# Kernel tuning notes

Hardware: AMD Instinct MI355X
Metric: run time of the kernel (lower is better)

Reference implementation:

```python
import jax, jax.numpy as jnp
import numpy as np

D = 384      # n_embed_dims
H = 6        # n_heads
HS = D // H  # head_size = 64
T = 256      # block_size
B = 256
EPS = 1e-5


def setup_inputs() -> dict:
    key = jax.random.key(0)
    ks = jax.random.split(key, 12)
    s_in = 1.0 / np.sqrt(D)
    s_ff = 1.0 / np.sqrt(4 * D)
    return {
        "x": jax.random.normal(ks[0], (B, T, D), jnp.float32),
        # per-head QKV weights, stacked [H, D, HS] (Linear bias=False)
        "wq": jax.random.normal(ks[1], (H, D, HS), jnp.float32) * s_in,
        "wk": jax.random.normal(ks[2], (H, D, HS), jnp.float32) * s_in,
        "wv": jax.random.normal(ks[3], (H, D, HS), jnp.float32) * s_in,
        "w_proj": jax.random.normal(ks[4], (D, D), jnp.float32) * s_in,
        "b_proj": jax.random.normal(ks[5], (D,), jnp.float32) * s_in,
        "w1": jax.random.normal(ks[6], (D, 4 * D), jnp.float32) * s_in,
        "b1": jax.random.normal(ks[7], (4 * D,), jnp.float32) * s_in,
        "w2": jax.random.normal(ks[8], (4 * D, D), jnp.float32) * s_ff,
        "b2": jax.random.normal(ks[9], (D,), jnp.float32) * s_ff,
        "g1": jnp.ones((D,), jnp.float32),
        "be1": jnp.zeros((D,), jnp.float32),
        "g2": jnp.ones((D,), jnp.float32),
        "be2": jnp.zeros((D,), jnp.float32),
    }


def _layernorm(x, g, b):
    mu = jnp.mean(x, axis=-1, keepdims=True)
    var = jnp.mean(jnp.square(x - mu), axis=-1, keepdims=True)
    return (x - mu) * jax.lax.rsqrt(var + EPS) * g + b


def _attention(x, wq, wk, wv, w_proj, b_proj):
    # faithful quirk: scale = 1/sqrt(C) with C = full embed dim (384)
    scale = 1.0 / jnp.sqrt(jnp.asarray(D, x.dtype))
    q = jnp.einsum("btd,hde->bhte", x, wq)  # [B,H,T,HS]
    k = jnp.einsum("btd,hde->bhte", x, wk)
    v = jnp.einsum("btd,hde->bhte", x, wv)
    w = jnp.einsum("bhte,bhse->bhts", q, k) * scale  # [B,H,T,T], no mask
    w = jax.nn.softmax(w, axis=-1)
    out = jnp.einsum("bhts,bhse->bhte", w, v)  # [B,H,T,HS]
    # concat heads along feature dim (head order matches torch cat)
    out = out.transpose(0, 2, 1, 3).reshape(x.shape[0], x.shape[1], D)
    return out @ w_proj + b_proj


def reference(x, wq, wk, wv, w_proj, b_proj, w1, b1, w2, b2, g1, be1, g2, be2):
    x = x + _attention(_layernorm(x, g1, be1), wq, wk, wv, w_proj, b_proj)
    h = _layernorm(x, g2, be2)
    h = jax.nn.relu(h @ w1 + b1) @ w2 + b2  # dropout = eval-mode identity
    return x + h
```

## Files before the change

### kernel.cpp

```cpp
#include <hip/hip_runtime.h>
#include <stdint.h>

#define NTOK 65536
#define DE 384
#define QSTR 1280

typedef __bf16 bf16x8 __attribute__((ext_vector_type(8)));
typedef float  f32x4 __attribute__((ext_vector_type(4)));
typedef unsigned short u16x8 __attribute__((ext_vector_type(8)));

__device__ __forceinline__ unsigned short f2bf(float f) {
  union { float fl; unsigned u; } a; a.fl = f;
  unsigned r = a.u + 0x7fffu + ((a.u >> 16) & 1u);
  return (unsigned short)(r >> 16);
}
__device__ __forceinline__ float b2f(unsigned short s) {
  union { unsigned u; float f; } v; v.u = (unsigned)s << 16; return v.f;
}

__device__ __forceinline__ void gll16(const void* g, void* l) {
  __builtin_amdgcn_global_load_lds((const __attribute__((address_space(1))) void*)g,
                                   (__attribute__((address_space(3))) void*)l, 16, 0, 0);
}

__device__ __forceinline__ bf16x8 ds128(unsigned addr) {
  bf16x8 r;
  asm volatile("ds_read_b128 %0, %1" : "=v"(r) : "v"(addr));
  return r;
}

__global__ void pack_t(unsigned short* __restrict__ dst, const float* __restrict__ src,
                       int R, int C) {
  int t = blockIdx.x * 256 + threadIdx.x;
  if (t >= R * C) return;
  int r = t / C, c = t - r * C;
  dst[(size_t)c * R + r] = f2bf(src[t]);
}

__global__ void qkv_pack(const float* __restrict__ wq, const float* __restrict__ wk,
                         const float* __restrict__ wv, unsigned short* __restrict__ dst) {
  int t = blockIdx.x * 256 + threadIdx.x;
  if (t >= QSTR * 384) return;
  int n = t / 384, k = t - n * 384;
  unsigned short v = 0;
  if (n < 1152) {
    int which = n / 384, r = n - which * 384;
    const float* src = which == 0 ? wq : (which == 1 ? wk : wv);
    int h = r >> 6, e = r & 63;
    v = f2bf(src[h * 24576 + k * 64 + e]);
  }
  dst[t] = v;
}

__global__ __launch_bounds__(256) void ln_kernel(const float* __restrict__ x,
                                                 const float* __restrict__ g,
                                                 const float* __restrict__ be,
                                                 unsigned short* __restrict__ out) {
  int wave = threadIdx.x >> 6, lane = threadIdx.x & 63;
  size_t row = (size_t)blockIdx.x * 4 + wave;
  const float* xr = x + row * DE;
  int c0 = lane * 2;
  float2 v0 = *(const float2*)(xr + c0);
  float2 v1 = *(const float2*)(xr + 128 + c0);
  float2 v2 = *(const float2*)(xr + 256 + c0);
  float s  = v0.x + v0.y + v1.x + v1.y + v2.x + v2.y;
  float ss = v0.x*v0.x + v0.y*v0.y + v1.x*v1.x + v1.y*v1.y + v2.x*v2.x + v2.y*v2.y;
#pragma unroll
  for (int m = 1; m < 64; m <<= 1) { s += __shfl_xor(s, m); ss += __shfl_xor(ss, m); }
  float mu = s * (1.0f / 384.0f);
  float rstd = rsqrtf(ss * (1.0f / 384.0f) - mu * mu + 1e-5f);
  unsigned short* orow = out + row * DE;
  {
    float a0 = (v0.x - mu) * rstd * g[c0] + be[c0];
    float a1 = (v0.y - mu) * rstd * g[c0 + 1] + be[c0 + 1];
    *(unsigned*)(orow + c0) = (unsigned)f2bf(a0) | ((unsigned)f2bf(a1) << 16);
  }
  {
    int c = c0 + 128;
    float a0 = (v1.x - mu) * rstd * g[c] + be[c];
    float a1 = (v1.y - mu) * rstd * g[c + 1] + be[c + 1];
    *(unsigned*)(orow + c) = (unsigned)f2bf(a0) | ((unsigned)f2bf(a1) << 16);
  }
  {
    int c = c0 + 256;
    float a0 = (v2.x - mu) * rstd * g[c] + be[c];
    float a1 = (v2.y - mu) * rstd * g[c + 1] + be[c + 1];
    *(unsigned*)(orow + c) = (unsigned)f2bf(a0) | ((unsigned)f2bf(a1) << 16);
  }
}

__global__ __launch_bounds__(256) void ln_bf16(const unsigned short* __restrict__ x,
                                               const float* __restrict__ g,
                                               const float* __restrict__ be,
                                               unsigned short* __restrict__ out) {
  int wave = threadIdx.x >> 6, lane = threadIdx.x & 63;
  size_t row = (size_t)blockIdx.x * 4 + wave;
  const unsigned short* xr = x + row * DE;
  int c0 = lane * 2;
  unsigned u0 = *(const unsigned*)(xr + c0);
  unsigned u1 = *(const unsigned*)(xr + 128 + c0);
  unsigned u2 = *(const unsigned*)(xr + 256 + c0);
  float a0 = b2f((unsigned short)u0), a1 = b2f((unsigned short)(u0 >> 16));
  float b0 = b2f((unsigned short)u1), b1 = b2f((unsigned short)(u1 >> 16));
  float d0 = b2f((unsigned short)u2), d1 = b2f((unsigned short)(u2 >> 16));
  float s  = a0 + a1 + b0 + b1 + d0 + d1;
  float ss = a0*a0 + a1*a1 + b0*b0 + b1*b1 + d0*d0 + d1*d1;
#pragma unroll
  for (int m = 1; m < 64; m <<= 1) { s += __shfl_xor(s, m); ss += __shfl_xor(ss, m); }
  float mu = s * (1.0f / 384.0f);
  float rstd = rsqrtf(ss * (1.0f / 384.0f) - mu * mu + 1e-5f);
  unsigned short* orow = out + row * DE;
  {
    float r0 = (a0 - mu) * rstd * g[c0] + be[c0];
    float r1 = (a1 - mu) * rstd * g[c0 + 1] + be[c0 + 1];
    *(unsigned*)(orow + c0) = (unsigned)f2bf(r0) | ((unsigned)f2bf(r1) << 16);
  }
  {
    int c = c0 + 128;
    float r0 = (b0 - mu) * rstd * g[c] + be[c];
    float r1 = (b1 - mu) * rstd * g[c + 1] + be[c + 1];
    *(unsigned*)(orow + c) = (unsigned)f2bf(r0) | ((unsigned)f2bf(r1) << 16);
  }
  {
    int c = c0 + 256;
    float r0 = (d0 - mu) * rstd * g[c] + be[c];
    float r1 = (d1 - mu) * rstd * g[c + 1] + be[c + 1];
    *(unsigned*)(orow + c) = (unsigned)f2bf(r0) | ((unsigned)f2bf(r1) << 16);
  }
}

template<int EPI, int BM, int BN, int WM, int WN>
__device__ __forceinline__
void gemm_core(const unsigned short* __restrict__ A, const unsigned short* __restrict__ Bt,
               int M, int Ncmp, int K, int Nst, int stride, int ntx,
               const float* __restrict__ bias, const float* __restrict__ residf,
               const unsigned short* __restrict__ residb,
               float* __restrict__ outf, unsigned short* __restrict__ outb) {
  constexpr int T = WM * WN * 64;
  constexpr int MWT = BM / WM, NWT = BN / WN;
  constexpr int MF = MWT / 16, NF = NWT / 16;
  constexpr int MH = MF / 4;
  constexpr int LA = (BM * 128) / (T * 16);
  constexpr int LB = (BN * 128) / (T * 16);
  __shared__ __align__(16) unsigned short As[2][BM * 64];
  __shared__ __align__(16) unsigned short Bs[2][BN * 64];
  const int tid = threadIdx.x;
  const int wave = tid >> 6, lane = tid & 63;

  const int nwg = gridDim.x;
  const int cpx = nwg >> 3;
  const int wg = (blockIdx.x & 7) * cpx + (blockIdx.x >> 3);
  const int bx = wg % ntx, by = wg / ntx;
  const int mBase = by * BM, nBase = bx * BN;
  const int wmi = wave / WN, wni = wave % WN;
  const int wm = wmi * MWT, wn = wni * NWT;
  const int fr = lane & 15, fg = lane >> 4;

  const unsigned asb = (unsigned)(uintptr_t)&As[0][0];
  const unsigned bsb = (unsigned)(uintptr_t)&Bs[0][0];

  f32x4 acc[MF][NF];
  const f32x4 z = {0.f, 0.f, 0.f, 0.f};
#pragma unroll
  for (int i = 0; i < MF; ++i)
#pragma unroll
    for (int j = 0; j < NF; ++j) acc[i][j] = z;

  auto stage = [&](int buf, int kt) {
#pragma unroll
    for (int i = 0; i < LA; ++i) {
      int Lb = i * (T * 16) + wave * 1024;
      int L = Lb + lane * 16;
      int row = L >> 7;
      int col = (((L >> 4) & 7) ^ (row & 7)) << 3;
      gll16(A + (size_t)(mBase + row) * K + kt + col, (unsigned short*)As[buf] + (Lb >> 1));
    }
#pragma unroll
    for (int i = 0; i < LB; ++i) {
      int Lb = i * (T * 16) + wave * 1024;
      int L = Lb + lane * 16;
      int row = L >> 7;
      int col = (((L >> 4) & 7) ^ (row & 7)) << 3;
      gll16(Bt + (size_t)(nBase + row) * K + kt + col, (unsigned short*)Bs[buf] + (Lb >> 1));
    }
  };

  const int NK = K >> 6;
  stage(0, 0);
  for (int t = 0; t < NK; ++t) {
    const int cur = t & 1;
    if (t + 1 < NK) {
      stage(cur ^ 1, (t + 1) << 6);
      if constexpr (LA + LB == 8) asm volatile("s_waitcnt vmcnt(8)" ::: "memory");
      else                        asm volatile("s_waitcnt vmcnt(6)" ::: "memory");
    } else {
      asm volatile("s_waitcnt vmcnt(0)" ::: "memory");
    }
    asm volatile("" ::: "memory");
    __builtin_amdgcn_s_barrier();
    asm volatile("" ::: "memory");

    const unsigned ab = asb + (cur ? (unsigned)(BM * 128) : 0u);
    const unsigned bb = bsb + (cur ? (unsigned)(BN * 128) : 0u);
#pragma unroll
    for (int ks = 0; ks < 2; ++ks) {
      bf16x8 bfr[NF];
#pragma unroll
      for (int nb = 0; nb < NF; ++nb) {
        int row = wn + nb * 16 + fr;
        unsigned byte = (unsigned)(row << 7) + ((unsigned)((ks * 4 + fg) ^ (row & 7)) << 4);
        bfr[nb] = ds128(bb + byte);
      }
#pragma unroll
      for (int mh = 0; mh < MH; ++mh) {
        bf16x8 af[4];
#pragma unroll
        for (int mb = 0; mb < 4; ++mb) {
          int row = wm + (mh * 4 + mb) * 16 + fr;
          unsigned byte = (unsigned)(row << 7) + ((unsigned)((ks * 4 + fg) ^ (row & 7)) << 4);
          af[mb] = ds128(ab + byte);
        }
        asm volatile("s_waitcnt lgkmcnt(0)" ::: "memory");
        __builtin_amdgcn_sched_barrier(0);
        __builtin_amdgcn_s_setprio(1);
#pragma unroll
        for (int mb = 0; mb < 4; ++mb)
#pragma unroll
          for (int nb = 0; nb < NF; ++nb)
            acc[mh * 4 + mb][nb] =
                __builtin_amdgcn_mfma_f32_16x16x32_bf16(af[mb], bfr[nb], acc[mh * 4 + mb][nb], 0, 0, 0);
        __builtin_amdgcn_s_setprio(0);
      }
    }
    asm volatile("" ::: "memory");
    __builtin_amdgcn_s_barrier();
    asm volatile("" ::: "memory");
  }

#pragma unroll
  for (int mb = 0; mb < MF; ++mb) {
#pragma unroll
    for (int nb = 0; nb < NF; ++nb) {
      const int gn = nBase + wn + nb * 16 + fr;
      if (gn < Nst) {
#pragma unroll
        for (int i = 0; i < 4; ++i) {
          const int gm = mBase + wm + mb * 16 + (fg << 2) + i;
          float val = acc[mb][nb][i];
          size_t idx = (size_t)gm * stride + gn;
          if (EPI == 0) {
            outb[idx] = f2bf(val);
          } else if (EPI == 1) {
            outb[idx] = f2bf(val + bias[gn] + residf[idx]);
          } else if (EPI == 2) {
            float r = val + bias[gn];
            outb[idx] = f2bf(r > 0.f ? r : 0.f);
          } else {
            outf[idx] = val + bias[gn] + b2f(residb[idx]);
          }
        }
      }
    }
  }
}

__global__ __launch_bounds__(512, 1)
void gemm_qkv(const unsigned short* __restrict__ A, const unsigned short* __restrict__ Bt,
              int M, int Ncmp, int K, int Nst, int stride, int ntx,
              const float* __restrict__ bias, const float* __restrict__ residf,
              const unsigned short* __restrict__ residb, float* __restrict__ outf,
              unsigned short* __restrict__ outb) {
  gemm_core<0, 256, 256, 2, 4>(A, Bt, M, Ncmp, K, Nst, stride, ntx, bias, residf, residb, outf, outb);
}
__global__ __launch_bounds__(512, 1)
void gemm_proj(const unsigned short* __restrict__ A, const unsigned short* __restrict__ Bt,
               int M, int Ncmp, int K, int Nst, int stride, int ntx,
               const float* __restrict__ bias, const float* __restrict__ residf,
               const unsigned short* __restrict__ residb, float* __restrict__ outf,
               unsigned short* __restrict__ outb) {
  gemm_core<1, 256, 128, 4, 2>(A, Bt, M, Ncmp, K, Nst, stride, ntx, bias, residf, residb, outf, outb);
}
__global__ __launch_bounds__(512, 1)
void gemm_mlp1(const unsigned short* __restrict__ A, const unsigned short* __restrict__ Bt,
               int M, int Ncmp, int K, int Nst, int stride, int ntx,
               const float* __restrict__ bias, const float* __restrict__ residf,
               const unsigned short* __restrict__ residb, float* __restrict__ outf,
               unsigned short* __restrict__ outb) {
  gemm_core<2, 256, 256, 2, 4>(A, Bt, M, Ncmp, K, Nst, stride, ntx, bias, residf, residb, outf, outb);
}
__global__ __launch_bounds__(512, 1)
void gemm_mlp2(const unsigned short* __restrict__ A, const unsigned short* __restrict__ Bt,
               int M, int Ncmp, int K, int Nst, int stride, int ntx,
               const float* __restrict__ bias, const float* __restrict__ residf,
               const unsigned short* __restrict__ residb, float* __restrict__ outf,
               unsigned short* __restrict__ outb) {
  gemm_core<3, 256, 128, 4, 2>(A, Bt, M, Ncmp, K, Nst, stride, ntx, bias, residf, residb, outf, outb);
}

__global__ __launch_bounds__(256)
void attn_kernel(const unsigned short* __restrict__ qkvn, unsigned short* __restrict__ o) {
  __shared__ unsigned short Vt[64 * 256];
  __shared__ unsigned short Pw[4][64 * 32];
  const int bh = blockIdx.x;
  const int b = bh / 6, h = bh - b * 6;
  const unsigned short* base = qkvn + (size_t)(b * 256) * QSTR;
  const unsigned short* qb = base + h * 64;
  const unsigned short* kbp = base + 384 + h * 64;
  const unsigned short* vbp = base + 768 + h * 64;
  const int wave = threadIdx.x >> 6, lane = threadIdx.x & 63;
  const int fr = lane & 15, fg = lane >> 4;
  const int fk = fg << 3;
  const int qrow0 = wave << 6;
  const float scale = 0.051031036307982884f;
  const f32x4 z = {0.f, 0.f, 0.f, 0.f};

  {
    const int s = threadIdx.x;
    u16x8 v8[8];
#pragma unroll
    for (int j = 0; j < 8; ++j)
      v8[j] = *(const u16x8*)(vbp + (size_t)s * QSTR + j * 8);
#pragma unroll
    for (int e = 0; e < 64; ++e)
      Vt[(e << 8) + (s ^ ((e & 7) << 3))] = v8[e >> 3][e & 7];
  }
  __syncthreads();

  bf16x8 qf[4][2];
#pragma unroll
  for (int rb = 0; rb < 4; ++rb)
#pragma unroll
    for (int ks = 0; ks < 2; ++ks)
      qf[rb][ks] = *(const bf16x8*)(qb + (size_t)(qrow0 + rb * 16 + fr) * QSTR + ks * 32 + fk);

  f32x4 oacc[4][4];
  float psum[4][4];
#pragma unroll
  for (int rb = 0; rb < 4; ++rb)
#pragma unroll
    for (int nb = 0; nb < 4; ++nb) oacc[rb][nb] = z;
#pragma unroll
  for (int rb = 0; rb < 4; ++rb)
#pragma unroll
    for (int i = 0; i < 4; ++i) psum[rb][i] = 0.f;

  for (int kb2 = 0; kb2 < 8; ++kb2) {
#pragma unroll
    for (int c2 = 0; c2 < 2; ++c2) {
      int cb = kb2 * 2 + c2;
      bf16x8 kf0 = *(const bf16x8*)(kbp + (size_t)(cb * 16 + fr) * QSTR + fk);
      bf16x8 kf1 = *(const bf16x8*)(kbp + (size_t)(cb * 16 + fr) * QSTR + 32 + fk);
#pragma unroll
      for (int rb = 0; rb < 4; ++rb) {
        f32x4 s = __builtin_amdgcn_mfma_f32_16x16x32_bf16(qf[rb][0], kf0, z, 0, 0, 0);
        s = __builtin_amdgcn_mfma_f32_16x16x32_bf16(qf[rb][1], kf1, s, 0, 0, 0);
#pragma unroll
        for (int i = 0; i < 4; ++i) {
          float p = __expf(fminf(scale * s[i], 60.f));
          psum[rb][i] += p;
          Pw[wave][(rb * 16 + (fg << 2) + i) * 32 + c2 * 16 + fr] = f2bf(p);
        }
      }
    }
    bf16x8 pa[4], vf[4];
#pragma unroll
    for (int rb = 0; rb < 4; ++rb) pa[rb] = *(const bf16x8*)(&Pw[wave][(rb * 16 + fr) * 32 + fk]);
#pragma unroll
    for (int nb = 0; nb < 4; ++nb) {
      int e = nb * 16 + fr;
      vf[nb] = *(const bf16x8*)(&Vt[(e << 8) + ((kb2 * 32 + fk) ^ ((e & 7) << 3))]);
    }
#pragma unroll
    for (int rb = 0; rb < 4; ++rb)
#pragma unroll
      for (int nb = 0; nb < 4; ++nb)
        oacc[rb][nb] = __builtin_amdgcn_mfma_f32_16x16x32_bf16(pa[rb], vf[nb], oacc[rb][nb], 0, 0, 0);
  }

  float rs[4][4];
#pragma unroll
  for (int rb = 0; rb < 4; ++rb)
#pragma unroll
    for (int i = 0; i < 4; ++i) {
      float v = psum[rb][i];
      v += __shfl_xor(v, 1);
      v += __shfl_xor(v, 2);
      v += __shfl_xor(v, 4);
      v += __shfl_xor(v, 8);
      rs[rb][i] = 1.0f / v;
    }

#pragma unroll
  for (int rb = 0; rb < 4; ++rb)
#pragma unroll
    for (int nb = 0; nb < 4; ++nb)
#pragma unroll
      for (int i = 0; i < 4; ++i) {
        int token = b * 256 + qrow0 + rb * 16 + (fg << 2) + i;
        int gcol = h * 64 + nb * 16 + fr;
        o[(size_t)token * DE + gcol] = f2bf(oacc[rb][nb][i] * rs[rb][i]);
      }
}

extern "C" void kernel_launch(void* const* d_in, const int* in_sizes, int n_in,
                              void* d_out, int out_size, void* d_ws, size_t ws_size,
                              hipStream_t stream) {
  const float* x     = (const float*)d_in[0];
  const float* wq    = (const float*)d_in[1];
  const float* wk    = (const float*)d_in[2];
  const float* wv    = (const float*)d_in[3];
  const float* wproj = (const float*)d_in[4];
  const float* bproj = (const float*)d_in[5];
  const float* w1    = (const float*)d_in[6];
  const float* b1    = (const float*)d_in[7];
  const float* w2    = (const float*)d_in[8];
  const float* b2    = (const float*)d_in[9];
  const float* g1    = (const float*)d_in[10];
  const float* be1   = (const float*)d_in[11];
  const float* g2    = (const float*)d_in[12];
  const float* be2   = (const float*)d_in[13];

  char* ws = (char*)d_ws;
  unsigned short* xln   = (unsigned short*)(ws + 0);
  unsigned short* x1b   = (unsigned short*)(ws + 0);
  unsigned short* qkvn  = (unsigned short*)(ws + 50331648);
  unsigned short* hbuf  = (unsigned short*)(ws + 100663296);
  unsigned short* act   = (unsigned short*)(ws + 150994944);
  unsigned short* attno = (unsigned short*)(ws + 218103808);
  unsigned short* wqkvt = (unsigned short*)(ws + 352321536);
  unsigned short* wprjt = (unsigned short*)(ws + 352321536 + 983040);
  unsigned short* w1t   = (unsigned short*)(ws + 352321536 + 983040 + 294912);
  unsigned short* w2t   = (unsigned short*)(ws + 352321536 + 983040 + 294912 + 1179648);

  qkv_pack<<<(QSTR * 384 + 255) / 256, 256, 0, stream>>>(wq, wk, wv, wqkvt);
  pack_t<<<(147456 + 255) / 256, 256, 0, stream>>>(wprjt, wproj, 384, 384);
  pack_t<<<(589824 + 255) / 256, 256, 0, stream>>>(w1t, w1, 384, 1536);
  pack_t<<<(589824 + 255) / 256, 256, 0, stream>>>(w2t, w2, 1536, 384);

  ln_kernel<<<NTOK / 4, 256, 0, stream>>>(x, g1, be1, xln);

  gemm_qkv<<<5 * 256, 512, 0, stream>>>(xln, wqkvt, NTOK, 1280, 384, 1152, 1280, 5,
                                        nullptr, nullptr, nullptr, nullptr, qkvn);

  attn_kernel<<<1536, 256, 0, stream>>>(qkvn, attno);

  gemm_proj<<<3 * 256, 512, 0, stream>>>(attno, wprjt, NTOK, 384, 384, 384, 384, 3,
                                         bproj, x, nullptr, nullptr, x1b);

  ln_bf16<<<NTOK / 4, 256, 0, stream>>>(x1b, g2, be2, hbuf);

  gemm_mlp1<<<6 * 256, 512, 0, stream>>>(hbuf, w1t, NTOK, 1536, 384, 1536, 1536, 6,
                                         b1, nullptr, nullptr, nullptr, act);

  gemm_mlp2<<<3 * 256, 512, 0, stream>>>(act, w2t, NTOK, 384, 1536, 384, 384, 3,
                                         b2, nullptr, x1b, (float*)d_out, nullptr);
}
```

Measured before the change: 544.4 us.

## Fuse second LayerNorm into projection GEMM epilogue and retile QKV GEMM

The projection GEMM now uses full-row tiles (BM=128, BN=384), so each workgroup holds complete rows. It adds bias and residual, computes the row mean and variance through shuffles and a shared-memory reduction, and writes both x1 and the LayerNorm-2 output. This removes the separate ln_bf16 kernel and its extra read of x1. The QKV GEMM tile width also changes from 256 to 192 columns, with 6 column tiles covering exactly 1152 instead of padding to 1280. In exchange, the projection grid drops to 512 workgroups with larger per-workgroup tiles, which risks lower occupancy and register pressure.

```diff
diff --git a/kernel.cpp b/kernel.cpp
--- a/kernel.cpp
+++ b/kernel.cpp
@@ -89,53 +89,15 @@
   }
 }
 
-__global__ __launch_bounds__(256) void ln_bf16(const unsigned short* __restrict__ x,
-                                               const float* __restrict__ g,
-                                               const float* __restrict__ be,
-                                               unsigned short* __restrict__ out) {
-  int wave = threadIdx.x >> 6, lane = threadIdx.x & 63;
-  size_t row = (size_t)blockIdx.x * 4 + wave;
-  const unsigned short* xr = x + row * DE;
-  int c0 = lane * 2;
-  unsigned u0 = *(const unsigned*)(xr + c0);
-  unsigned u1 = *(const unsigned*)(xr + 128 + c0);
-  unsigned u2 = *(const unsigned*)(xr + 256 + c0);
-  float a0 = b2f((unsigned short)u0), a1 = b2f((unsigned short)(u0 >> 16));
-  float b0 = b2f((unsigned short)u1), b1 = b2f((unsigned short)(u1 >> 16));
-  float d0 = b2f((unsigned short)u2), d1 = b2f((unsigned short)(u2 >> 16));
-  float s  = a0 + a1 + b0 + b1 + d0 + d1;
-  float ss = a0*a0 + a1*a1 + b0*b0 + b1*b1 + d0*d0 + d1*d1;
-#pragma unroll
-  for (int m = 1; m < 64; m <<= 1) { s += __shfl_xor(s, m); ss += __shfl_xor(ss, m); }
-  float mu = s * (1.0f / 384.0f);
-  float rstd = rsqrtf(ss * (1.0f / 384.0f) - mu * mu + 1e-5f);
-  unsigned short* orow = out + row * DE;
-  {
-    float r0 = (a0 - mu) * rstd * g[c0] + be[c0];
-    float r1 = (a1 - mu) * rstd * g[c0 + 1] + be[c0 + 1];
-    *(unsigned*)(orow + c0) = (unsigned)f2bf(r0) | ((unsigned)f2bf(r1) << 16);
-  }
-  {
-    int c = c0 + 128;
-    float r0 = (b0 - mu) * rstd * g[c] + be[c];
-    float r1 = (b1 - mu) * rstd * g[c + 1] + be[c + 1];
-    *(unsigned*)(orow + c) = (unsigned)f2bf(r0) | ((unsigned)f2bf(r1) << 16);
-  }
-  {
-    int c = c0 + 256;
-    float r0 = (d0 - mu) * rstd * g[c] + be[c];
-    float r1 = (d1 - mu) * rstd * g[c + 1] + be[c + 1];
-    *(unsigned*)(orow + c) = (unsigned)f2bf(r0) | ((unsigned)f2bf(r1) << 16);
-  }
-}
-
 template<int EPI, int BM, int BN, int WM, int WN>
 __device__ __forceinline__
 void gemm_core(const unsigned short* __restrict__ A, const unsigned short* __restrict__ Bt,
-               int M, int Ncmp, int K, int Nst, int stride, int ntx,
+               int M, int K, int Nst, int stride, int ntx,
                const float* __restrict__ bias, const float* __restrict__ residf,
                const unsigned short* __restrict__ residb,
-               float* __restrict__ outf, unsigned short* __restrict__ outb) {
+               const float* __restrict__ g2, const float* __restrict__ be2,
+               float* __restrict__ outf, unsigned short* __restrict__ outb,
+               unsigned short* __restrict__ out2) {
   constexpr int T = WM * WN * 64;
   constexpr int MWT = BM / WM, NWT = BN / WN;
   constexpr int MF = MWT / 16, NF = NWT / 16;
@@ -144,6 +106,7 @@
   constexpr int LB = (BN * 128) / (T * 16);
   __shared__ __align__(16) unsigned short As[2][BM * 64];
   __shared__ __align__(16) unsigned short Bs[2][BN * 64];
+  __shared__ float red[BM][4][2];
   const int tid = threadIdx.x;
   const int wave = tid >> 6, lane = tid & 63;
 
@@ -191,8 +154,9 @@
     const int cur = t & 1;
     if (t + 1 < NK) {
       stage(cur ^ 1, (t + 1) << 6);
-      if constexpr (LA + LB == 8) asm volatile("s_waitcnt vmcnt(8)" ::: "memory");
-      else                        asm volatile("s_waitcnt vmcnt(6)" ::: "memory");
+      if constexpr (LA + LB == 8)      asm volatile("s_waitcnt vmcnt(8)" ::: "memory");
+      else if constexpr (LA + LB == 7) asm volatile("s_waitcnt vmcnt(7)" ::: "memory");
+      else                             asm volatile("s_waitcnt vmcnt(6)" ::: "memory");
     } else {
       asm volatile("s_waitcnt vmcnt(0)" ::: "memory");
     }
@@ -235,6 +199,65 @@
     asm volatile("" ::: "memory");
     __builtin_amdgcn_s_barrier();
     asm volatile("" ::: "memory");
+  }
+
+  if (EPI == 1) {
+#pragma unroll
+    for (int mb = 0; mb < MF; ++mb) {
+#pragma unroll
+      for (int nb = 0; nb < NF; ++nb) {
+        const int gn = nBase + wn + nb * 16 + fr;
+#pragma unroll
+        for (int i = 0; i < 4; ++i) {
+          const int gm = mBase + wm + mb * 16 + (fg << 2) + i;
+          size_t idx = (size_t)gm * stride + gn;
+          acc[mb][nb][i] = acc[mb][nb][i] + bias[gn] + residf[idx];
+        }
+      }
+    }
+#pragma unroll
+    for (int mb = 0; mb < MF; ++mb) {
+#pragma unroll
+      for (int i = 0; i < 4; ++i) {
+        float s = 0.f, ss = 0.f;
+#pragma unroll
+        for (int nb = 0; nb < NF; ++nb) {
+          float v = acc[mb][nb][i];
+          s += v; ss += v * v;
+        }
+        s += __shfl_xor(s, 1); ss += __shfl_xor(ss, 1);
+        s += __shfl_xor(s, 2); ss += __shfl_xor(ss, 2);
+        s += __shfl_xor(s, 4); ss += __shfl_xor(ss, 4);
+        s += __shfl_xor(s, 8); ss += __shfl_xor(ss, 8);
+        if (fr == 0) {
+          int row = wm + mb * 16 + (fg << 2) + i;
+          red[row][wni][0] = s;
+          red[row][wni][1] = ss;
+        }
+      }
+    }
+    __syncthreads();
+#pragma unroll
+    for (int mb = 0; mb < MF; ++mb) {
+#pragma unroll
+      for (int i = 0; i < 4; ++i) {
+        int row = wm + mb * 16 + (fg << 2) + i;
+        float s = red[row][0][0] + red[row][1][0] + red[row][2][0] + red[row][3][0];
+        float ss = red[row][0][1] + red[row][1][1] + red[row][2][1] + red[row][3][1];
+        float mu = s * (1.0f / 384.0f);
+        float rstd = rsqrtf(ss * (1.0f / 384.0f) - mu * mu + 1e-5f);
+        const int gm = mBase + row;
+#pragma unroll
+        for (int nb = 0; nb < NF; ++nb) {
+          const int gn = nBase + wn + nb * 16 + fr;
+          size_t idx = (size_t)gm * stride + gn;
+          float x1v = acc[mb][nb][i];
+          outb[idx] = f2bf(x1v);
+          out2[idx] = f2bf((x1v - mu) * rstd * g2[gn] + be2[gn]);
+        }
+      }
+    }
+    return;
   }
 
 #pragma unroll
@@ -250,8 +273,6 @@
           size_t idx = (size_t)gm * stride + gn;
           if (EPI == 0) {
             outb[idx] = f2bf(val);
-          } else if (EPI == 1) {
-            outb[idx] = f2bf(val + bias[gn] + residf[idx]);
           } else if (EPI == 2) {
             float r = val + bias[gn];
             outb[idx] = f2bf(r > 0.f ? r : 0.f);
@@ -266,35 +287,39 @@
 
 __global__ __launch_bounds__(512, 1)
 void gemm_qkv(const unsigned short* __restrict__ A, const unsigned short* __restrict__ Bt,
-              int M, int Ncmp, int K, int Nst, int stride, int ntx,
+              int M, int K, int Nst, int stride, int ntx,
               const float* __restrict__ bias, const float* __restrict__ residf,
               const unsigned short* __restrict__ residb, float* __restrict__ outf,
               unsigned short* __restrict__ outb) {
-  gemm_core<0, 256, 256, 2, 4>(A, Bt, M, Ncmp, K, Nst, stride, ntx, bias, residf, residb, outf, outb);
+  gemm_core<0, 256, 192, 2, 4>(A, Bt, M, K, Nst, stride, ntx, bias, residf, residb,
+                               nullptr, nullptr, outf, outb, nullptr);
 }
 __global__ __launch_bounds__(512, 1)
-void gemm_proj(const unsigned short* __restrict__ A, const unsigned short* __restrict__ Bt,
-               int M, int Ncmp, int K, int Nst, int stride, int ntx,
+void gemm_projln(const unsigned short* __restrict__ A, const unsigned short* __restrict__ Bt,
+                 int M, int K, int Nst, int stride, int ntx,
+                 const float* __restrict__ bias, const float* __restrict__ residf,
+                 const float* __restrict__ g2, const float* __restrict__ be2,
+                 unsigned short* __restrict__ outb, unsigned short* __restrict__ out2) {
+  gemm_core<1, 128, 384, 2, 4>(A, Bt, M, K, Nst, stride, ntx, bias, residf, nullptr,
+                               g2, be2, nullptr, outb, out2);
+}
+__global__ __launch_bounds__(512, 1)
+void gemm_mlp1(const unsigned short* __restrict__ A, const unsigned short* __restrict__ Bt,
+               int M, int K, int Nst, int stride, int ntx,
                const float* __restrict__ bias, const float* __restrict__ residf,
                const unsigned short* __restrict__ residb, float* __restrict__ outf,
                unsigned short* __restrict__ outb) {
-  gemm_core<1, 256, 128, 4, 2>(A, Bt, M, Ncmp, K, Nst, stride, ntx, bias, residf, residb, outf, outb);
+  gemm_core<2, 256, 256, 2, 4>(A, Bt, M, K, Nst, stride, ntx, bias, residf, residb,
+                               nullptr, nullptr, outf, outb, nullptr);
 }
 __global__ __launch_bounds__(512, 1)
-void gemm_mlp1(const unsigned short* __restrict__ A, const unsigned short* __restrict__ Bt,
-               int M, int Ncmp, int K, int Nst, int stride, int ntx,
+void gemm_mlp2(const unsigned short* __restrict__ A, const unsigned short* __restrict__ Bt,
+               int M, int K, int Nst, int stride, int ntx,
                const float* __restrict__ bias, const float* __restrict__ residf,
                const unsigned short* __restrict__ residb, float* __restrict__ outf,
                unsigned short* __restrict__ outb) {
-  gemm_core<2, 256, 256, 2, 4>(A, Bt, M, Ncmp, K, Nst, stride, ntx, bias, residf, residb, outf, outb);
-}
-__global__ __launch_bounds__(512, 1)
-void gemm_mlp2(const unsigned short* __restrict__ A, const unsigned short* __restrict__ Bt,
-               int M, int Ncmp, int K, int Nst, int stride, int ntx,
-               const float* __restrict__ bias, const float* __restrict__ residf,
-               const unsigned short* __restrict__ residb, float* __restrict__ outf,
-               unsigned short* __restrict__ outb) {
-  gemm_core<3, 256, 128, 4, 2>(A, Bt, M, Ncmp, K, Nst, stride, ntx, bias, residf, residb, outf, outb);
+  gemm_core<3, 256, 128, 4, 2>(A, Bt, M, K, Nst, stride, ntx, bias, residf, residb,
+                               nullptr, nullptr, outf, outb, nullptr);
 }
 
 __global__ __launch_bounds__(256)
@@ -439,19 +464,17 @@
 
   ln_kernel<<<NTOK / 4, 256, 0, stream>>>(x, g1, be1, xln);
 
-  gemm_qkv<<<5 * 256, 512, 0, stream>>>(xln, wqkvt, NTOK, 1280, 384, 1152, 1280, 5,
+  gemm_qkv<<<6 * 256, 512, 0, stream>>>(xln, wqkvt, NTOK, 384, 1152, 1280, 6,
                                         nullptr, nullptr, nullptr, nullptr, qkvn);
 
   attn_kernel<<<1536, 256, 0, stream>>>(qkvn, attno);
 
-  gemm_proj<<<3 * 256, 512, 0, stream>>>(attno, wprjt, NTOK, 384, 384, 384, 384, 3,
-                                         bproj, x, nullptr, nullptr, x1b);
-
-  ln_bf16<<<NTOK / 4, 256, 0, stream>>>(x1b, g2, be2, hbuf);
-
-  gemm_mlp1<<<6 * 256, 512, 0, stream>>>(hbuf, w1t, NTOK, 1536, 384, 1536, 1536, 6,
+  gemm_projln<<<512, 512, 0, stream>>>(attno, wprjt, NTOK, 384, 384, 384, 1,
+                                       bproj, x, g2, be2, x1b, hbuf);
+
+  gemm_mlp1<<<6 * 256, 512, 0, stream>>>(hbuf, w1t, NTOK, 384, 1536, 1536, 6,
                                          b1, nullptr, nullptr, nullptr, act);
 
-  gemm_mlp2<<<3 * 256, 512, 0, stream>>>(act, w2t, NTOK, 384, 1536, 384, 384, 3,
+  gemm_mlp2<<<3 * 256, 512, 0, stream>>>(act, w2t, NTOK, 1536, 384, 384, 3,
                                          b2, nullptr, x1b, (float*)d_out, nullptr);
 }
```

Result: faster. 530.0 us (-2.6%).
